# Kernel optimization log

Hardware: AMD Instinct MI355X
Metric: run time of the kernel (lower is better)

Reference implementation:

```python
import jax, jax.numpy as jnp
import numpy as np

N_NODES = 100000
N_CHANNELS = 64
N_EDGES = 1200000
K_CHEB = 6


def _cheb_norm(edge_index, num_nodes):
    # PyG ChebConv sym normalization with lambda_max=2.0:
    # L_hat = 2L/lambda_max - I = -D^{-1/2} A D^{-1/2} (diagonal becomes 0)
    row, col = edge_index[0], edge_index[1]
    ones = jnp.ones(edge_index.shape[1], dtype=jnp.float32)
    deg = jax.ops.segment_sum(ones, row, num_segments=num_nodes)
    dinv = jnp.where(deg > 0, jax.lax.rsqrt(jnp.where(deg > 0, deg, 1.0)), 0.0)
    norm = -dinv[row] * dinv[col]  # [E]
    return norm


def _propagate(x, row, col, norm, num_nodes):
    # out[i] = sum_{e: row[e]==i} norm[e] * x[col[e]]
    msgs = norm[:, None] * x[col]  # [E, C]
    return jax.ops.segment_sum(msgs, row, num_segments=num_nodes)


def _cheb_conv(x, W, b, row, col, norm, num_nodes):
    # W: [K, C_in, C_out]; Chebyshev recursion T0=x, T1=Lhat x, Tk=2 Lhat T_{k-1}-T_{k-2}
    Tx0 = x
    out = Tx0 @ W[0]
    Tx1 = _propagate(Tx0, row, col, norm, num_nodes)
    out = out + Tx1 @ W[1]
    for k in range(2, W.shape[0]):
        Tx2 = 2.0 * _propagate(Tx1, row, col, norm, num_nodes) - Tx0
        out = out + Tx2 @ W[k]
        Tx0, Tx1 = Tx1, Tx2
    return out + b


def setup_inputs() -> dict:
    key = jax.random.key(0)
    ks = jax.random.split(key, 8)
    pos = jax.random.normal(ks[0], (N_NODES, N_CHANNELS), dtype=jnp.float32)
    edge_index = jax.random.randint(ks[1], (2, N_EDGES), 0, N_NODES, dtype=jnp.int64)
    scale = 1.0 / np.sqrt(N_CHANNELS)
    W1 = jax.random.normal(ks[2], (K_CHEB, N_CHANNELS, N_CHANNELS), dtype=jnp.float32) * scale
    W2 = jax.random.normal(ks[3], (K_CHEB, N_CHANNELS, N_CHANNELS), dtype=jnp.float32) * scale
    W3 = jax.random.normal(ks[4], (K_CHEB, N_CHANNELS, N_CHANNELS), dtype=jnp.float32) * scale
    b1 = jnp.zeros((N_CHANNELS,), dtype=jnp.float32)
    b2 = jnp.zeros((N_CHANNELS,), dtype=jnp.float32)
    b3 = jnp.zeros((N_CHANNELS,), dtype=jnp.float32)
    return {"pos": pos, "edge_index": edge_index,
            "W1": W1, "b1": b1, "W2": W2, "b2": b2, "W3": W3, "b3": b3}


def reference(pos, edge_index, W1, b1, W2, b2, W3, b3):
    num_nodes = pos.shape[0]
    row, col = edge_index[0], edge_index[1]
    norm = _cheb_norm(edge_index, num_nodes)
    residual = pos
    h = jax.nn.relu(_cheb_conv(pos, W1, b1, row, col, norm, num_nodes))
    h = jax.nn.relu(_cheb_conv(h, W2, b2, row, col, norm, num_nodes))
    h = jax.nn.relu(_cheb_conv(h, W3, b3, row, col, norm, num_nodes))
    return h + residual
```

## Files before the change

kernel.cpp:

```cpp
#include <hip/hip_runtime.h>
#include <hip/hip_bf16.h>
#include <math.h>

#define NN 100000
#define NE 1200000
#define NC 64
#define NB 391
#define NTILE 6250

typedef unsigned short u16;
typedef __attribute__((ext_vector_type(8))) short short8;
typedef __attribute__((ext_vector_type(4))) float f32x4;

__device__ __forceinline__ float bf2f(u16 u) {
    return __uint_as_float(((unsigned)u) << 16);
}
__device__ __forceinline__ u16 f2bf(float f) {
    __hip_bfloat16 h = __float2bfloat16(f);
    return *reinterpret_cast<u16*>(&h);
}

__global__ __launch_bounds__(256) void deg_kernel(const int* __restrict__ ei, int* __restrict__ deg) {
    int e = blockIdx.x * 256 + threadIdx.x;
    if (e < NE) atomicAdd(&deg[ei[e]], 1);
}

__global__ __launch_bounds__(256) void scan1_kernel(const int* __restrict__ deg,
                                                    int* __restrict__ tmp,
                                                    int* __restrict__ bsum) {
    __shared__ int s[256];
    int i = blockIdx.x * 256 + threadIdx.x;
    int v = (i < NN) ? deg[i] : 0;
    s[threadIdx.x] = v;
    __syncthreads();
    for (int off = 1; off < 256; off <<= 1) {
        int t = (threadIdx.x >= off) ? s[threadIdx.x - off] : 0;
        __syncthreads();
        s[threadIdx.x] += t;
        __syncthreads();
    }
    if (i < NN) tmp[i] = s[threadIdx.x];
    if (threadIdx.x == 255) bsum[blockIdx.x] = s[255];
}

__global__ __launch_bounds__(512) void scan2_kernel(const int* __restrict__ bsum,
                                                    int* __restrict__ boff) {
    __shared__ int s[512];
    int t = threadIdx.x;
    int v = (t < NB) ? bsum[t] : 0;
    s[t] = v;
    __syncthreads();
    for (int off = 1; off < 512; off <<= 1) {
        int u = (t >= off) ? s[t - off] : 0;
        __syncthreads();
        s[t] += u;
        __syncthreads();
    }
    if (t < NB) boff[t] = s[t] - v;
}

__global__ __launch_bounds__(256) void scan3_kernel(const int* __restrict__ deg,
                                                    const int* __restrict__ tmp,
                                                    const int* __restrict__ boff,
                                                    int* __restrict__ row_ptr,
                                                    float* __restrict__ dinv) {
    int i = blockIdx.x * 256 + threadIdx.x;
    if (i >= NN) return;
    int d = deg[i];
    int start = tmp[i] - d + boff[blockIdx.x];
    row_ptr[i] = start;
    dinv[i] = (d > 0) ? rsqrtf((float)d) : 0.f;
    if (i == NN - 1) row_ptr[NN] = start + d;
}

__global__ __launch_bounds__(256) void fill_kernel(const int* __restrict__ ei,
                                                   const int* __restrict__ row_ptr,
                                                   int* __restrict__ cnt,
                                                   const float* __restrict__ dinv,
                                                   int2* __restrict__ csr) {
    int e = blockIdx.x * 256 + threadIdx.x;
    if (e >= NE) return;
    int r = ei[e];
    int c = ei[NE + e];
    int p = atomicAdd(&cnt[r], 1);
    csr[row_ptr[r] + p] = make_int2(c, (int)__float_as_uint(dinv[c]));
}

__global__ __launch_bounds__(256) void wcat_kernel(const float* __restrict__ W1,
                                                   const float* __restrict__ W2,
                                                   const float* __restrict__ W3,
                                                   u16* __restrict__ WT) {
    int idx = blockIdx.x * 256 + threadIdx.x;
    if (idx >= 3 * 64 * 384) return;
    int l = idx / (64 * 384);
    int rem = idx - l * (64 * 384);
    int co = rem / 384;
    int kk = rem - co * 384;
    const float* W = (l == 0) ? W1 : ((l == 1) ? W2 : W3);
    WT[idx] = f2bf(W[kk * 64 + co]);
}

__global__ __launch_bounds__(256) void cvt_kernel(const float4* __restrict__ in,
                                                  ushort4* __restrict__ outb, int n4) {
    int i = blockIdx.x * 256 + threadIdx.x;
    if (i < n4) {
        float4 v = in[i];
        ushort4 u;
        u.x = f2bf(v.x); u.y = f2bf(v.y); u.z = f2bf(v.z); u.w = f2bf(v.w);
        outb[i] = u;
    }
}

template <bool FIRST>
__global__ __launch_bounds__(256, 6) void prop_kernel(
    const u16* __restrict__ t0, const u16* __restrict__ t1, u16* __restrict__ t2,
    const int2* __restrict__ csr, const int* __restrict__ row_ptr,
    const float* __restrict__ dinv) {
    int lane = threadIdx.x & 63;
    int wid = __builtin_amdgcn_readfirstlane((int)(threadIdx.x >> 6));
    int base = (blockIdx.x * 4 + wid) * 4;

    int sN[4], dN[4];
    int2 ce[4];
#pragma unroll
    for (int n = 0; n < 4; ++n) {
        int i = base + n;
        sN[n] = row_ptr[i];
        dN[n] = row_ptr[i + 1] - sN[n];
        ce[n] = make_int2(0, 0);
        if (dN[n] > 0) ce[n] = csr[sN[n] + min(lane, dN[n] - 1)];
    }

    float dv[4], x0[4];
#pragma unroll
    for (int n = 0; n < 4; ++n) {
        dv[n] = dinv[base + n];
        x0[n] = 0.f;
        if (!FIRST) x0[n] = bf2f(t0[(size_t)(base + n) * 64 + lane]);
    }

    int kmax = max(max(min(dN[0], 64), min(dN[1], 64)),
                   max(min(dN[2], 64), min(dN[3], 64)));

    float acc[4] = {0.f, 0.f, 0.f, 0.f};
#pragma unroll 4
    for (int k = 0; k < kmax; ++k) {
#pragma unroll
        for (int n = 0; n < 4; ++n) {
            int col = __builtin_amdgcn_readlane(ce[n].x, k);
            float w = __uint_as_float((unsigned)__builtin_amdgcn_readlane(ce[n].y, k));
            w = (k < dN[n]) ? w : 0.f;
            acc[n] = fmaf(w, bf2f(t1[(size_t)col * 64 + lane]), acc[n]);
        }
    }

#pragma unroll
    for (int n = 0; n < 4; ++n) {
        for (int b = 64; b < dN[n]; b += 64) {
            int rem = min(dN[n] - b, 64);
            int2 c2 = csr[sN[n] + b + min(lane, rem - 1)];
            for (int k = 0; k < rem; ++k) {
                int col = __builtin_amdgcn_readlane(c2.x, k);
                float w = __uint_as_float((unsigned)__builtin_amdgcn_readlane(c2.y, k));
                acc[n] = fmaf(w, bf2f(t1[(size_t)col * 64 + lane]), acc[n]);
            }
        }
    }

#pragma unroll
    for (int n = 0; n < 4; ++n) {
        float p = -dv[n] * acc[n];
        float v = FIRST ? p : fmaf(2.f, p, -x0[n]);
        t2[(size_t)(base + n) * 64 + lane] = f2bf(v);
    }
}

template <int MODE>
__global__ __launch_bounds__(256) void gemm_kernel(
    const u16* __restrict__ T0, const u16* __restrict__ T1, const u16* __restrict__ T2,
    const u16* __restrict__ T3, const u16* __restrict__ T4, const u16* __restrict__ T5,
    const u16* __restrict__ WT, const float* __restrict__ bias,
    u16* __restrict__ xout, float* __restrict__ fout, const float* __restrict__ pos) {
    int lane = threadIdx.x & 63;
    int wid = __builtin_amdgcn_readfirstlane((int)(threadIdx.x >> 6));
    int tile = blockIdx.x * 4 + wid;
    if (tile >= NTILE) return;
    int r = lane & 15;
    int kg = lane >> 4;
    int arow = tile * 16 + r;

    f32x4 acc[4];
#pragma unroll
    for (int t = 0; t < 4; ++t) {
        float b = bias[t * 16 + r];
        acc[t] = (f32x4){b, b, b, b};
    }

    const u16* Ts[6] = {T0, T1, T2, T3, T4, T5};
#pragma unroll
    for (int kb = 0; kb < 6; ++kb) {
        const u16* Tb = Ts[kb];
        short8 a0 = *(const short8*)(Tb + (size_t)arow * 64 + kg * 8);
        short8 a1 = *(const short8*)(Tb + (size_t)arow * 64 + 32 + kg * 8);
#pragma unroll
        for (int t = 0; t < 4; ++t) {
            const u16* wb = WT + (size_t)(t * 16 + r) * 384 + kb * 64 + kg * 8;
            short8 b0 = *(const short8*)(wb);
            short8 b1 = *(const short8*)(wb + 32);
            acc[t] = __builtin_amdgcn_mfma_f32_16x16x32_bf16(a0, b0, acc[t], 0, 0, 0);
            acc[t] = __builtin_amdgcn_mfma_f32_16x16x32_bf16(a1, b1, acc[t], 0, 0, 0);
        }
    }

#pragma unroll
    for (int t = 0; t < 4; ++t) {
#pragma unroll
        for (int rr = 0; rr < 4; ++rr) {
            int row = tile * 16 + kg * 4 + rr;
            int col = t * 16 + r;
            float v = acc[t][rr];
            if (MODE == 0) {
                xout[(size_t)row * 64 + col] = f2bf(fmaxf(v, 0.f));
            } else {
                fout[(size_t)row * 64 + col] = fmaxf(v, 0.f) + pos[(size_t)row * 64 + col];
            }
        }
    }
}

extern "C" void kernel_launch(void* const* d_in, const int* in_sizes, int n_in,
                              void* d_out, int out_size, void* d_ws, size_t ws_size,
                              hipStream_t stream) {
    const float* pos = (const float*)d_in[0];
    const int* ei = (const int*)d_in[1];
    const float* W1 = (const float*)d_in[2];
    const float* b1 = (const float*)d_in[3];
    const float* W2 = (const float*)d_in[4];
    const float* b2 = (const float*)d_in[5];
    const float* W3 = (const float*)d_in[6];
    const float* b3 = (const float*)d_in[7];
    float* out = (float*)d_out;

    char* ws = (char*)d_ws;
    size_t off = 0;
    auto alloc = [&](size_t bytes) {
        void* p = ws + off;
        off += (bytes + 1023) & ~(size_t)1023;
        return p;
    };
    int* deg = (int*)alloc(NN * 4);
    float* dinv = (float*)alloc(NN * 4);
    int* row_ptr = (int*)alloc((NN + 1) * 4);
    int* cnt = (int*)alloc(NN * 4);
    int* tmp = (int*)alloc(NN * 4);
    int* bsum = (int*)alloc(NB * 4);
    int* boff = (int*)alloc(NB * 4);
    int2* csr = (int2*)alloc((size_t)NE * 8);
    u16* WT = (u16*)alloc((size_t)3 * 64 * 384 * 2);
    u16* X = (u16*)alloc((size_t)NN * NC * 2);
    u16* T1 = (u16*)alloc((size_t)NN * NC * 2);
    u16* T2 = (u16*)alloc((size_t)NN * NC * 2);
    u16* T3 = (u16*)alloc((size_t)NN * NC * 2);
    u16* T4 = (u16*)alloc((size_t)NN * NC * 2);
    u16* T5 = (u16*)alloc((size_t)NN * NC * 2);

    hipMemsetAsync(deg, 0, NN * 4, stream);
    hipMemsetAsync(cnt, 0, NN * 4, stream);
    deg_kernel<<<(NE + 255) / 256, 256, 0, stream>>>(ei, deg);
    scan1_kernel<<<NB, 256, 0, stream>>>(deg, tmp, bsum);
    scan2_kernel<<<1, 512, 0, stream>>>(bsum, boff);
    scan3_kernel<<<NB, 256, 0, stream>>>(deg, tmp, boff, row_ptr, dinv);
    fill_kernel<<<(NE + 255) / 256, 256, 0, stream>>>(ei, row_ptr, cnt, dinv, csr);
    wcat_kernel<<<(3 * 64 * 384 + 255) / 256, 256, 0, stream>>>(W1, W2, W3, WT);

    const int G = NN / 16;
    const int G4 = (NN * NC / 4) / 256;
    const int GG = (NTILE + 3) / 4;

    cvt_kernel<<<G4, 256, 0, stream>>>((const float4*)pos, (ushort4*)X, NN * NC / 4);

    prop_kernel<true><<<G, 256, 0, stream>>>(X, X, T1, csr, row_ptr, dinv);
    prop_kernel<false><<<G, 256, 0, stream>>>(X, T1, T2, csr, row_ptr, dinv);
    prop_kernel<false><<<G, 256, 0, stream>>>(T1, T2, T3, csr, row_ptr, dinv);
    prop_kernel<false><<<G, 256, 0, stream>>>(T2, T3, T4, csr, row_ptr, dinv);
    prop_kernel<false><<<G, 256, 0, stream>>>(T3, T4, T5, csr, row_ptr, dinv);
    gemm_kernel<0><<<GG, 256, 0, stream>>>(X, T1, T2, T3, T4, T5, WT, b1, X, nullptr, nullptr);

    prop_kernel<true><<<G, 256, 0, stream>>>(X, X, T1, csr, row_ptr, dinv);
    prop_kernel<false><<<G, 256, 0, stream>>>(X, T1, T2, csr, row_ptr, dinv);
    prop_kernel<false><<<G, 256, 0, stream>>>(T1, T2, T3, csr, row_ptr, dinv);
    prop_kernel<false><<<G, 256, 0, stream>>>(T2, T3, T4, csr, row_ptr, dinv);
    prop_kernel<false><<<G, 256, 0, stream>>>(T3, T4, T5, csr, row_ptr, dinv);
    gemm_kernel<0><<<GG, 256, 0, stream>>>(X, T1, T2, T3, T4, T5, WT + 24576, b2, X, nullptr, nullptr);

    prop_kernel<true><<<G, 256, 0, stream>>>(X, X, T1, csr, row_ptr, dinv);
    prop_kernel<false><<<G, 256, 0, stream>>>(X, T1, T2, csr, row_ptr, dinv);
    prop_kernel<false><<<G, 256, 0, stream>>>(T1, T2, T3, csr, row_ptr, dinv);
    prop_kernel<false><<<G, 256, 0, stream>>>(T2, T3, T4, csr, row_ptr, dinv);
    prop_kernel<false><<<G, 256, 0, stream>>>(T3, T4, T5, csr, row_ptr, dinv);
    gemm_kernel<1><<<GG, 256, 0, stream>>>(X, T1, T2, T3, T4, T5, WT + 2 * 24576, b3, nullptr, out, pos);
}
```

Before: 894.5 us.

## Gather two edges per wave with 32-bit loads and record slot positions in degree pass

In the propagation kernel, each half-wave now handles a different edge, and each lane loads a packed pair of bf16 channels as one 32-bit word. This halves the gather instructions per edge, and the two halves are combined with a cross-lane shuffle at the end. Separately, the degree kernel stores each edge's atomic slot index, so the CSR fill no longer needs a second atomic pass or a memset of the counter array. In exchange it adds a 4.8MB position buffer plus extra shuffle and select work.

```diff
diff --git a/kernel.cpp b/kernel.cpp
--- a/kernel.cpp
+++ b/kernel.cpp
@@ -20,9 +20,11 @@
     return *reinterpret_cast<u16*>(&h);
 }
 
-__global__ __launch_bounds__(256) void deg_kernel(const int* __restrict__ ei, int* __restrict__ deg) {
+__global__ __launch_bounds__(256) void deg_kernel(const int* __restrict__ ei,
+                                                  int* __restrict__ deg,
+                                                  int* __restrict__ ppos) {
     int e = blockIdx.x * 256 + threadIdx.x;
-    if (e < NE) atomicAdd(&deg[ei[e]], 1);
+    if (e < NE) ppos[e] = atomicAdd(&deg[ei[e]], 1);
 }
 
 __global__ __launch_bounds__(256) void scan1_kernel(const int* __restrict__ deg,
@@ -75,15 +77,14 @@
 
 __global__ __launch_bounds__(256) void fill_kernel(const int* __restrict__ ei,
                                                    const int* __restrict__ row_ptr,
-                                                   int* __restrict__ cnt,
+                                                   const int* __restrict__ ppos,
                                                    const float* __restrict__ dinv,
                                                    int2* __restrict__ csr) {
     int e = blockIdx.x * 256 + threadIdx.x;
     if (e >= NE) return;
     int r = ei[e];
     int c = ei[NE + e];
-    int p = atomicAdd(&cnt[r], 1);
-    csr[row_ptr[r] + p] = make_int2(c, (int)__float_as_uint(dinv[c]));
+    csr[row_ptr[r] + ppos[e]] = make_int2(c, (int)__float_as_uint(dinv[c]));
 }
 
 __global__ __launch_bounds__(256) void wcat_kernel(const float* __restrict__ W1,
@@ -119,6 +120,8 @@
     int lane = threadIdx.x & 63;
     int wid = __builtin_amdgcn_readfirstlane((int)(threadIdx.x >> 6));
     int base = (blockIdx.x * 4 + wid) * 4;
+    int half = lane >> 5;
+    int ch2 = lane & 31;
 
     int sN[4], dN[4];
     int2 ce[4];
@@ -131,26 +134,34 @@
         if (dN[n] > 0) ce[n] = csr[sN[n] + min(lane, dN[n] - 1)];
     }
 
-    float dv[4], x0[4];
+    float dv[4];
+    unsigned x0u[4];
 #pragma unroll
     for (int n = 0; n < 4; ++n) {
         dv[n] = dinv[base + n];
-        x0[n] = 0.f;
-        if (!FIRST) x0[n] = bf2f(t0[(size_t)(base + n) * 64 + lane]);
+        x0u[n] = 0u;
+        if (!FIRST) x0u[n] = *(const unsigned*)(t0 + (size_t)(base + n) * 64 + ch2 * 2);
     }
 
     int kmax = max(max(min(dN[0], 64), min(dN[1], 64)),
                    max(min(dN[2], 64), min(dN[3], 64)));
 
-    float acc[4] = {0.f, 0.f, 0.f, 0.f};
+    float acc0[4] = {0.f, 0.f, 0.f, 0.f};
+    float acc1[4] = {0.f, 0.f, 0.f, 0.f};
 #pragma unroll 4
-    for (int k = 0; k < kmax; ++k) {
+    for (int k = 0; k < kmax; k += 2) {
 #pragma unroll
         for (int n = 0; n < 4; ++n) {
-            int col = __builtin_amdgcn_readlane(ce[n].x, k);
-            float w = __uint_as_float((unsigned)__builtin_amdgcn_readlane(ce[n].y, k));
-            w = (k < dN[n]) ? w : 0.f;
-            acc[n] = fmaf(w, bf2f(t1[(size_t)col * 64 + lane]), acc[n]);
+            int colA = __builtin_amdgcn_readlane(ce[n].x, k);
+            int colB = __builtin_amdgcn_readlane(ce[n].x, k + 1);
+            float wA = __uint_as_float((unsigned)__builtin_amdgcn_readlane(ce[n].y, k));
+            float wB = __uint_as_float((unsigned)__builtin_amdgcn_readlane(ce[n].y, k + 1));
+            int col = half ? colB : colA;
+            float w = half ? wB : wA;
+            w = ((k + half) < dN[n]) ? w : 0.f;
+            unsigned v = *(const unsigned*)(t1 + (size_t)col * 64 + ch2 * 2);
+            acc0[n] = fmaf(w, __uint_as_float(v << 16), acc0[n]);
+            acc1[n] = fmaf(w, __uint_as_float(v & 0xffff0000u), acc1[n]);
         }
     }
 
@@ -159,19 +170,38 @@
         for (int b = 64; b < dN[n]; b += 64) {
             int rem = min(dN[n] - b, 64);
             int2 c2 = csr[sN[n] + b + min(lane, rem - 1)];
-            for (int k = 0; k < rem; ++k) {
-                int col = __builtin_amdgcn_readlane(c2.x, k);
-                float w = __uint_as_float((unsigned)__builtin_amdgcn_readlane(c2.y, k));
-                acc[n] = fmaf(w, bf2f(t1[(size_t)col * 64 + lane]), acc[n]);
+            for (int k = 0; k < rem; k += 2) {
+                int colA = __builtin_amdgcn_readlane(c2.x, k);
+                int colB = __builtin_amdgcn_readlane(c2.x, min(k + 1, 63));
+                float wA = __uint_as_float((unsigned)__builtin_amdgcn_readlane(c2.y, k));
+                float wB = __uint_as_float((unsigned)__builtin_amdgcn_readlane(c2.y, min(k + 1, 63)));
+                int col = half ? colB : colA;
+                float w = half ? wB : wA;
+                w = ((k + half) < rem) ? w : 0.f;
+                unsigned v = *(const unsigned*)(t1 + (size_t)col * 64 + ch2 * 2);
+                acc0[n] = fmaf(w, __uint_as_float(v << 16), acc0[n]);
+                acc1[n] = fmaf(w, __uint_as_float(v & 0xffff0000u), acc1[n]);
             }
         }
     }
 
 #pragma unroll
     for (int n = 0; n < 4; ++n) {
-        float p = -dv[n] * acc[n];
-        float v = FIRST ? p : fmaf(2.f, p, -x0[n]);
-        t2[(size_t)(base + n) * 64 + lane] = f2bf(v);
+        float s0 = acc0[n] + __shfl_xor(acc0[n], 32);
+        float s1 = acc1[n] + __shfl_xor(acc1[n], 32);
+        float p0 = -dv[n] * s0;
+        float p1 = -dv[n] * s1;
+        float v0, v1;
+        if (FIRST) {
+            v0 = p0; v1 = p1;
+        } else {
+            v0 = fmaf(2.f, p0, -__uint_as_float(x0u[n] << 16));
+            v1 = fmaf(2.f, p1, -__uint_as_float(x0u[n] & 0xffff0000u));
+        }
+        if (half == 0) {
+            unsigned o = (unsigned)f2bf(v0) | ((unsigned)f2bf(v1) << 16);
+            *(unsigned*)(t2 + (size_t)(base + n) * 64 + ch2 * 2) = o;
+        }
     }
 }
 
@@ -251,10 +281,10 @@
     int* deg = (int*)alloc(NN * 4);
     float* dinv = (float*)alloc(NN * 4);
     int* row_ptr = (int*)alloc((NN + 1) * 4);
-    int* cnt = (int*)alloc(NN * 4);
     int* tmp = (int*)alloc(NN * 4);
     int* bsum = (int*)alloc(NB * 4);
     int* boff = (int*)alloc(NB * 4);
+    int* ppos = (int*)alloc((size_t)NE * 4);
     int2* csr = (int2*)alloc((size_t)NE * 8);
     u16* WT = (u16*)alloc((size_t)3 * 64 * 384 * 2);
     u16* X = (u16*)alloc((size_t)NN * NC * 2);
@@ -265,12 +295,11 @@
     u16* T5 = (u16*)alloc((size_t)NN * NC * 2);
 
     hipMemsetAsync(deg, 0, NN * 4, stream);
-    hipMemsetAsync(cnt, 0, NN * 4, stream);
-    deg_kernel<<<(NE + 255) / 256, 256, 0, stream>>>(ei, deg);
+    deg_kernel<<<(NE + 255) / 256, 256, 0, stream>>>(ei, deg, ppos);
     scan1_kernel<<<NB, 256, 0, stream>>>(deg, tmp, bsum);
     scan2_kernel<<<1, 512, 0, stream>>>(bsum, boff);
     scan3_kernel<<<NB, 256, 0, stream>>>(deg, tmp, boff, row_ptr, dinv);
-    fill_kernel<<<(NE + 255) / 256, 256, 0, stream>>>(ei, row_ptr, cnt, dinv, csr);
+    fill_kernel<<<(NE + 255) / 256, 256, 0, stream>>>(ei, row_ptr, ppos, dinv, csr);
     wcat_kernel<<<(3 * 64 * 384 + 255) / 256, 256, 0, stream>>>(W1, W2, W3, WT);
 
     const int G = NN / 16;
```

New measurement: 892.7 us. Within noise of the previous version (-0.2%).
